# Performance work log

Hardware: AMD Instinct MI355X
Metric: run time of the kernel (lower is better)

Reference implementation:

```python
import jax, jax.numpy as jnp
import numpy as np

N_SRC = 200000   # layer-0 source frontier (nodes)
N_E0  = 100000   # layer-0 targets (hyperedges)
N_E1  = 50000    # layer-1 targets
E0    = 1000000  # edges in layer 0
E1    = 500000   # edges in layer 1
D     = 128      # embedding_dim
H     = 8        # attn heads
BETA  = 0.5      # residual_beta
SLOPE = 0.2      # leaky-relu negative slope
BN_EPS = 1e-5


def _params(key):
    ks = jax.random.split(key, 12)
    def w(k):
        return jax.random.normal(k, (D, D), dtype=jnp.float32) * 0.05
    p = {}
    for i, nm in enumerate(['v2e_Wq', 'v2e_Wk', 'v2e_Wv', 'v2e_We', 'v2e_Wskip',
                            'e2rel_Wq', 'e2rel_Wk', 'e2rel_Wv', 'e2rel_We', 'e2rel_Wskip']):
        p[nm] = w(ks[i])
    p['bn_gamma'] = jnp.ones((D,), jnp.float32)
    p['bn_beta'] = jnp.zeros((D,), jnp.float32)
    return p


def setup_inputs() -> dict:
    key = jax.random.key(0)
    ks = jax.random.split(key, 8)
    inp = {
        'x': jax.random.normal(ks[0], (N_SRC, D), dtype=jnp.float32),
        'ei0': jnp.stack([jax.random.randint(ks[1], (E0,), 0, N_SRC),
                          jax.random.randint(ks[2], (E0,), 0, N_E0)]).astype(jnp.int32),
        'et0': jax.random.randint(ks[3], (E0,), 0, 4).astype(jnp.int32),
        'ei1': jnp.stack([jax.random.randint(ks[4], (E1,), 0, N_E0),
                          jax.random.randint(ks[5], (E1,), 0, N_E1)]).astype(jnp.int32),
        'et1': jax.random.randint(ks[6], (E1,), 0, 4).astype(jnp.int32),
        'emb_type': jax.random.normal(ks[7], (4, D), dtype=jnp.float32),
        'emb_attr': jax.random.normal(jax.random.fold_in(key, 99), (4, D), dtype=jnp.float32),
    }
    inp.update(_params(jax.random.fold_in(key, 1)))
    return inp


def ht_conv(x_src, x_dst, ei, ek, ev, Wq, Wk, Wv, We, Wskip):
    """HypergraphTransformer conv: multi-head edge attention + residual skip.
    x_src [Ns,D], x_dst [Nd,D], ei [2,E], ek/ev [E,D] edge-type/attr embeds."""
    Nd = x_dst.shape[0]
    d = D // H
    src, dst = ei[0], ei[1]
    q = (x_dst @ Wq).reshape(Nd, H, d)                    # [Nd,H,d]
    k = (x_src @ Wk).reshape(-1, H, d)[src] + (ek @ We).reshape(-1, H, d)  # [E,H,d]
    v = (x_src @ Wv).reshape(-1, H, d)[src] + (ev @ We).reshape(-1, H, d)  # [E,H,d]
    logits = jnp.einsum('ehd,ehd->eh', q[dst], k) / jnp.sqrt(jnp.float32(d))
    logits = jnp.where(logits >= 0, logits, SLOPE * logits)  # leaky relu
    # segment softmax over edges sharing a destination
    m = jax.ops.segment_max(logits, dst, num_segments=Nd)    # [Nd,H]
    a = jnp.exp(logits - m[dst])
    s = jax.ops.segment_sum(a, dst, num_segments=Nd)
    alpha = a / (s[dst] + 1e-16)                             # [E,H]
    out = jax.ops.segment_sum(alpha[..., None] * v, dst, num_segments=Nd)  # [Nd,H,d]
    out = out.reshape(Nd, D)
    return BETA * (x_dst @ Wskip) + (1.0 - BETA) * out


def batch_norm(x, gamma, beta):
    mu = jnp.mean(x, axis=0)
    var = jnp.var(x, axis=0)
    return (x - mu) * jax.lax.rsqrt(var + BN_EPS) * gamma + beta


def reference(x, ei0, et0, ei1, et1, emb_type, emb_attr,
              v2e_Wq, v2e_Wk, v2e_Wv, v2e_We, v2e_Wskip,
              e2rel_Wq, e2rel_Wk, e2rel_Wv, e2rel_We, e2rel_Wskip,
              bn_gamma, bn_beta):
    # layer 0: v2e + BatchNorm
    h = ht_conv(x, x[:N_E0], ei0, emb_type[et0], emb_attr[et0],
                v2e_Wq, v2e_Wk, v2e_Wv, v2e_We, v2e_Wskip)
    h = batch_norm(h, bn_gamma, bn_beta)
    # layer 1 (last): e2rel, no BN
    out = ht_conv(h, h[:N_E1], ei1, emb_type[et1], emb_attr[et1],
                  e2rel_Wq, e2rel_Wk, e2rel_Wv, e2rel_We, e2rel_Wskip)
    return out
```

## Files before the change

kernel.cpp:

```cpp
#include <hip/hip_runtime.h>
#include <cstdint>
#include <cstddef>

#define D 128
#define H 8
#define NSRC 200000
#define NE0  100000
#define NE1  50000
#define E0N  1000000
#define E1N  500000
#define NT   (NE0 + NE1)
#define ET   (E0N + E1N)

typedef unsigned short u16;
typedef __attribute__((ext_vector_type(8))) short short8;
typedef __attribute__((ext_vector_type(4))) float f32x4;
typedef __attribute__((ext_vector_type(2))) float f32x2;

__device__ __forceinline__ u16 f2bf(float f) {
  unsigned u = __float_as_uint(f);
  unsigned r = (u + 0x7fffu + ((u >> 16) & 1u)) >> 16;
  return (u16)r;
}
__device__ __forceinline__ float bf2f(u16 u) {
  return __uint_as_float(((unsigned)u) << 16);
}
__device__ __forceinline__ f32x2 unpk(unsigned u) {
  f32x2 r;
  r.x = __uint_as_float(u << 16);
  r.y = __uint_as_float(u & 0xffff0000u);
  return r;
}
__device__ __forceinline__ float dot2bf(unsigned a, unsigned b, float c) {
  float d;
  asm("v_dot2_f32_bf16 %0, %1, %2, %3" : "=v"(d) : "v"(a), "v"(b), "v"(c));
  return d;
}
__device__ __forceinline__ f32x2 fma2(f32x2 a, f32x2 b, f32x2 c) {
  return __builtin_elementwise_fma(a, b, c);
}

#define BC 25000
#define BZ 147
static_assert((size_t)BZ * 1024 >= NT + 1, "offs zero-fill must cover NT+1 entries");
__global__ __launch_bounds__(256) void prep_all(
    const float* __restrict__ x, u16* __restrict__ xb,
    const float* w0, const float* w1, const float* w2, const float* w3,
    const float* w4, const float* w5, const float* w6, const float* w7,
    u16* __restrict__ wt,
    const float* __restrict__ embA, const float* __restrict__ embB,
    const float* __restrict__ We0, const float* __restrict__ We1,
    float* __restrict__ kv,
    int* __restrict__ offs, float* __restrict__ bnsums) {
  int b = blockIdx.x;
  if (b < BC) {
    int i = b * 256 + threadIdx.x;
    float4 a = ((const float4*)x)[i];
    ushort4 o;
    o.x = f2bf(a.x); o.y = f2bf(a.y); o.z = f2bf(a.z); o.w = f2bf(a.w);
    ((ushort4*)xb)[i] = o;
  } else if (b < BC + 64) {
    int bb = b - BC;
    const float* wsrc[8] = {w0, w1, w2, w3, w4, w5, w6, w7};
    int mat = bb >> 3;
    int blk = bb & 7;
    const float* W = wsrc[mat];
    float sc = ((mat & 3) == 2) ? 0.25f : 1.0f;
    u16* out = wt + mat * 16384;
    for (int i = blk * 2048 + threadIdx.x; i < (blk + 1) * 2048; i += 256) {
      int n = i >> 7, k = i & 127;
      out[i] = f2bf(W[k * 128 + n] * sc);
    }
  } else if (b < BC + 68) {
    int bb = b - BC - 64;
    int mat = bb >> 1;
    int t = (bb & 1) * 256 + threadIdx.x;
    const float* We = mat ? We1 : We0;
    float* keOut = kv + mat * 1024;
    float* veOut = keOut + 512;
    int r = t >> 7, c = t & 127;
    float s0 = 0.f, s1 = 0.f;
    for (int k = 0; k < 128; ++k) {
      float w = We[k * 128 + c];
      s0 += embA[r * 128 + k] * w;
      s1 += embB[r * 128 + k] * w;
    }
    keOut[t] = s0;
    veOut[t] = s1;
  } else if (b < BC + 68 + BZ) {
    int base = (b - BC - 68) * 1024 + threadIdx.x * 4;
#pragma unroll
    for (int i = 0; i < 4; ++i)
      if (base + i < NT + 1) offs[base + i] = 0;
  } else {
    bnsums[threadIdx.x] = 0.f;
  }
}

__global__ __launch_bounds__(512, 4) void gemm_quad(
    const u16* __restrict__ A,
    const u16* __restrict__ WtK, const u16* __restrict__ WtV,
    u16* __restrict__ CKV, int NA, int nKV,
    const u16* __restrict__ WtQ, const u16* __restrict__ WtS,
    u16* __restrict__ CQ, u16* __restrict__ CS, int NB) {
  int bb = blockIdx.x;
  const u16 *Wt0, *Wt1;
  int N, tile0;
  bool ilv = (bb < nKV);
  if (ilv) {
    Wt0 = WtK; Wt1 = WtV; N = NA; tile0 = bb * 128;
  } else {
    Wt0 = WtQ; Wt1 = WtS; N = NB; tile0 = (bb - nKV) * 128;
  }
  int tid = threadIdx.x;
  int w = tid >> 6, lane = tid & 63;
  int g = w >> 1;
  int h = w & 1;
  int lrow = lane & 15, q = lane >> 4;

  __shared__ u16 Wls[2 * 128 * 128];

  uint4 wv[8];
#pragma unroll
  for (int i = 0; i < 8; ++i) {
    int m = i * 512 + tid;
    const u16* Wsrc = (m >> 11) ? Wt1 : Wt0;
    wv[i] = *(const uint4*)(Wsrc + (size_t)(m & 2047) * 8);
  }

  int ra = tile0 + g * 32 + lrow;
  int rb = ra + 16;
  bool oka = ra < N, okb = rb < N;
  const u16* pa = A + (size_t)(oka ? ra : 0) * 128 + q * 8;
  const u16* pb = A + (size_t)(okb ? rb : 0) * 128 + q * 8;
  short8 av[4], bv[4];
#pragma unroll
  for (int kk = 0; kk < 4; ++kk) {
    av[kk] = *(const short8*)(pa + kk * 32);
    bv[kk] = *(const short8*)(pb + kk * 32);
  }

#pragma unroll
  for (int i = 0; i < 8; ++i) {
    int m = i * 512 + tid;
    int row = (m & 2047) >> 4, c = m & 15;
    *(uint4*)(Wls + (m >> 11) * 16384 + row * 128 + (c ^ (row & 15)) * 8) = wv[i];
  }
  __syncthreads();

  const u16* W0 = Wls + (h * 64) * 128;
  const u16* W1 = Wls + 16384 + (h * 64) * 128;

  f32x4 acc[2][2][4];
#pragma unroll
  for (int o = 0; o < 2; ++o)
#pragma unroll
    for (int i = 0; i < 2; ++i)
#pragma unroll
      for (int j = 0; j < 4; ++j) acc[o][i][j] = (f32x4){0.f, 0.f, 0.f, 0.f};

  const short8 zero8 = {0, 0, 0, 0, 0, 0, 0, 0};
#pragma unroll
  for (int kk = 0; kk < 4; ++kk) {
    short8 a0 = oka ? av[kk] : zero8;
    short8 a1 = okb ? bv[kk] : zero8;
    int cs = ((kk * 4 + q) ^ lrow) * 8;
#pragma unroll
    for (int j = 0; j < 4; ++j) {
      int fr = j * 16 + lrow;
      short8 b0 = *(const short8*)(W0 + fr * 128 + cs);
      short8 b1 = *(const short8*)(W1 + fr * 128 + cs);
      acc[0][0][j] = __builtin_amdgcn_mfma_f32_16x16x32_bf16(b0, a0, acc[0][0][j], 0, 0, 0);
      acc[0][1][j] = __builtin_amdgcn_mfma_f32_16x16x32_bf16(b0, a1, acc[0][1][j], 0, 0, 0);
      acc[1][0][j] = __builtin_amdgcn_mfma_f32_16x16x32_bf16(b1, a0, acc[1][0][j], 0, 0, 0);
      acc[1][1][j] = __builtin_amdgcn_mfma_f32_16x16x32_bf16(b1, a1, acc[1][1][j], 0, 0, 0);
    }
  }

  if (ilv) {
#pragma unroll
    for (int i = 0; i < 2; ++i) {
      int grow = tile0 + g * 32 + i * 16 + lrow;
      if (grow < N) {
#pragma unroll
        for (int o = 0; o < 2; ++o) {
          u16* base = CKV + (size_t)grow * 256 + (o << 3) + ((q & 1) << 2) +
                      ((q >> 1) << 4) + h * 128;
#pragma unroll
          for (int j = 0; j < 4; ++j) {
            f32x4 v = acc[o][i][j];
            ushort4 pk;
            pk.x = f2bf(v[0]); pk.y = f2bf(v[1]); pk.z = f2bf(v[2]); pk.w = f2bf(v[3]);
            *(ushort4*)(base + j * 32) = pk;
          }
        }
      }
    }
  } else {
#pragma unroll
    for (int o = 0; o < 2; ++o) {
      u16* C = o ? CS : CQ;
#pragma unroll
      for (int i = 0; i < 2; ++i) {
        int grow = tile0 + g * 32 + i * 16 + lrow;
        if (grow < N) {
          u16* base = C + (size_t)grow * 128 + q * 4 + h * 64;
#pragma unroll
          for (int j = 0; j < 4; ++j) {
            f32x4 v = acc[o][i][j];
            ushort4 pk;
            pk.x = f2bf(v[0]); pk.y = f2bf(v[1]); pk.z = f2bf(v[2]); pk.w = f2bf(v[3]);
            *(ushort4*)(base + j * 16) = pk;
          }
        }
      }
    }
  }
}

__global__ __launch_bounds__(256) void csr_count2(
    const int* __restrict__ dst0, const int* __restrict__ dst1,
    int* __restrict__ cnt, int* __restrict__ rank) {
  int t = blockIdx.x * 256 + threadIdx.x;
  if (t < E0N) {
    rank[t] = atomicAdd(&cnt[dst0[t]], 1);
  } else if (t < ET) {
    rank[t] = atomicAdd(&cnt[NE0 + dst1[t - E0N]], 1);
  }
}

__global__ __launch_bounds__(256) void scan1(const int* __restrict__ cnt,
                                             int* __restrict__ excl,
                                             int* __restrict__ blocksums, int N) {
  __shared__ int sh[256];
  int tid = threadIdx.x;
  int base = blockIdx.x * 1024 + tid * 4;
  int v0 = (base + 0 < N) ? cnt[base + 0] : 0;
  int v1 = (base + 1 < N) ? cnt[base + 1] : 0;
  int v2 = (base + 2 < N) ? cnt[base + 2] : 0;
  int v3 = (base + 3 < N) ? cnt[base + 3] : 0;
  int tsum = v0 + v1 + v2 + v3;
  sh[tid] = tsum;
  __syncthreads();
  for (int off = 1; off < 256; off <<= 1) {
    int t2 = (tid >= off) ? sh[tid - off] : 0;
    __syncthreads();
    sh[tid] += t2;
    __syncthreads();
  }
  int incl = sh[tid];
  if (tid == 255) blocksums[blockIdx.x] = incl;
  int run = incl - tsum;
  if (base + 0 < N) excl[base + 0] = run; run += v0;
  if (base + 1 < N) excl[base + 1] = run; run += v1;
  if (base + 2 < N) excl[base + 2] = run; run += v2;
  if (base + 3 < N) excl[base + 3] = run;
}

__global__ void scan2(int* __restrict__ blocksums, int nb) {
  __shared__ int sh[256];
  int tid = threadIdx.x;
  int v = (tid < nb) ? blocksums[tid] : 0;
  sh[tid] = v;
  __syncthreads();
  for (int off = 1; off < 256; off <<= 1) {
    int t2 = (tid >= off) ? sh[tid - off] : 0;
    __syncthreads();
    sh[tid] += t2;
    __syncthreads();
  }
  if (tid < nb) blocksums[tid] = sh[tid] - v;
}

__global__ __launch_bounds__(256) void scan3(int* __restrict__ offs,
                                             const int* __restrict__ blocksums, int N,
                                             int Etot) {
  int t = blockIdx.x * 256 + threadIdx.x;
  if (t < N) offs[t] += blocksums[t >> 10];
  if (t == 0) offs[N] = Etot;
}

__global__ __launch_bounds__(256) void csr_fill2(
    const int* __restrict__ dst0, const int* __restrict__ src0, const int* __restrict__ et0,
    const int* __restrict__ dst1, const int* __restrict__ src1, const int* __restrict__ et1,
    const int* __restrict__ offs, const int* __restrict__ rank,
    int* __restrict__ elist) {
  int t = blockIdx.x * 256 + threadIdx.x;
  if (t < E0N) {
    int p = offs[dst0[t]] + rank[t];
    elist[p] = (src0[t] << 2) | et0[t];
  } else if (t < ET) {
    int t2 = t - E0N;
    int p = offs[NE0 + dst1[t2]] + rank[t];
    elist[p] = (src1[t2] << 2) | et1[t2];
  }
}

__device__ __forceinline__ float sel4(float s0, float s1, float s2, float s3, int ty) {
  float a = (ty & 1) ? s1 : s0;
  float b = (ty & 1) ? s3 : s2;
  return (ty & 2) ? b : a;
}

#define ATTN_BLOCKS 1024

__global__ __launch_bounds__(256) void attn_fused(
    const int* __restrict__ elist, const int* __restrict__ offs,
    const u16* __restrict__ Q, const u16* __restrict__ KV,
    const float* __restrict__ ke, const float* __restrict__ ve,
    const u16* __restrict__ skipb, float* __restrict__ outp, int N,
    float* __restrict__ bnsums) {
  int lane = threadIdx.x & 63;
  int wid = (blockIdx.x << 2) + (threadIdx.x >> 6);
  int wstride = gridDim.x << 2;
  int which = lane >> 4;
  int sub = lane & 15;
  int dim0 = sub * 8;
  int sub16 = sub * 16;
  bool dosum = (bnsums != nullptr);

  __shared__ float vels[4 * 136];
  __shared__ float bsum[128], bsq[128];
  for (int i = threadIdx.x; i < 512; i += 256) {
    int t = i >> 7, c = i & 127;
    vels[t * 136 + c] = ve[t * 128 + c];
  }
  if (threadIdx.x < 128) {
    bsum[threadIdx.x] = 0.f;
    bsq[threadIdx.x] = 0.f;
  }
  __syncthreads();

  float ls[8], lq[8];
#pragma unroll
  for (int i = 0; i < 8; ++i) { ls[i] = 0.f; lq[i] = 0.f; }

  for (int grp = wid; grp * 4 < N; grp += wstride) {
    int d = grp * 4 + which;
    bool active = d < N;
    int dc = active ? d : 0;

    uint4 qp = *(const uint4*)(Q + (size_t)dc * D + dim0);
    f32x2 u0 = unpk(qp.x), u1 = unpk(qp.y), u2 = unpk(qp.z), u3 = unpk(qp.w);

    float qk0, qk1, qk2, qk3;
#pragma unroll
    for (int ty = 0; ty < 4; ++ty) {
      const float* kt = ke + ty * D + dim0;
      float4 ka = *(const float4*)kt;
      float4 kb = *(const float4*)(kt + 4);
      float p = u0.x * ka.x + u0.y * ka.y + u1.x * ka.z + u1.y * ka.w +
                u2.x * kb.x + u2.y * kb.y + u3.x * kb.z + u3.y * kb.w;
      p += __shfl_xor(p, 1, 64);
      if (ty == 0) qk0 = p; else if (ty == 1) qk1 = p; else if (ty == 2) qk2 = p; else qk3 = p;
    }

    int j0 = active ? offs[d] : 0;
    int j1 = active ? offs[d + 1] : 0;
    int j = j0;

    int cp0, cp1, cp2, cp3;
    int fp0, fp1, fp2, fp3;
    {
      int i0 = (j + 0 < j1) ? j + 0 : 0;
      int i1 = (j + 1 < j1) ? j + 1 : 0;
      int i2 = (j + 2 < j1) ? j + 2 : 0;
      int i3 = (j + 3 < j1) ? j + 3 : 0;
      cp0 = elist[i0]; cp1 = elist[i1]; cp2 = elist[i2]; cp3 = elist[i3];
      int k0 = (j + 4 < j1) ? j + 4 : 0;
      int k1 = (j + 5 < j1) ? j + 5 : 0;
      int k2 = (j + 6 < j1) ? j + 6 : 0;
      int k3 = (j + 7 < j1) ? j + 7 : 0;
      fp0 = elist[k0]; fp1 = elist[k1]; fp2 = elist[k2]; fp3 = elist[k3];
    }
    uint4 ck0 = *(const uint4*)(KV + (size_t)(cp0 >> 2) * 256 + sub16);
    uint4 ck1 = *(const uint4*)(KV + (size_t)(cp1 >> 2) * 256 + sub16);
    uint4 ck2 = *(const uint4*)(KV + (size_t)(cp2 >> 2) * 256 + sub16);
    uint4 ck3 = *(const uint4*)(KV + (size_t)(cp3 >> 2) * 256 + sub16);
    uint4 cw0 = *(const uint4*)(KV + (size_t)(cp0 >> 2) * 256 + sub16 + 8);
    uint4 cw1 = *(const uint4*)(KV + (size_t)(cp1 >> 2) * 256 + sub16 + 8);
    uint4 cw2 = *(const uint4*)(KV + (size_t)(cp2 >> 2) * 256 + sub16 + 8);
    uint4 cw3 = *(const uint4*)(KV + (size_t)(cp3 >> 2) * 256 + sub16 + 8);

    float m = -INFINITY, s = 0.f;
    f32x2 acc01 = {0.f, 0.f}, acc23 = {0.f, 0.f}, acc45 = {0.f, 0.f}, acc67 = {0.f, 0.f};

    while (__any(j < j1)) {
      int jn = j + 4;
      uint4 nk0 = *(const uint4*)(KV + (size_t)(fp0 >> 2) * 256 + sub16);
      uint4 nk1 = *(const uint4*)(KV + (size_t)(fp1 >> 2) * 256 + sub16);
      uint4 nk2 = *(const uint4*)(KV + (size_t)(fp2 >> 2) * 256 + sub16);
      uint4 nk3 = *(const uint4*)(KV + (size_t)(fp3 >> 2) * 256 + sub16);
      uint4 nw0 = *(const uint4*)(KV + (size_t)(fp0 >> 2) * 256 + sub16 + 8);
      uint4 nw1 = *(const uint4*)(KV + (size_t)(fp1 >> 2) * 256 + sub16 + 8);
      uint4 nw2 = *(const uint4*)(KV + (size_t)(fp2 >> 2) * 256 + sub16 + 8);
      uint4 nw3 = *(const uint4*)(KV + (size_t)(fp3 >> 2) * 256 + sub16 + 8);
      int g0 = (jn + 4 < j1) ? jn + 4 : 0;
      int g1 = (jn + 5 < j1) ? jn + 5 : 0;
      int g2 = (jn + 6 < j1) ? jn + 6 : 0;
      int g3 = (jn + 7 < j1) ? jn + 7 : 0;
      int gp0 = elist[g0], gp1 = elist[g1], gp2 = elist[g2], gp3 = elist[g3];

      int n = j1 - j;
      if (n > 0) {
        int t0 = cp0 & 3, t1 = cp1 & 3, t2 = cp2 & 3, t3 = cp3 & 3;
        const float* vp0 = vels + t0 * 136 + dim0;
        const float* vp1 = vels + t1 * 136 + dim0;
        const float* vp2 = vels + t2 * 136 + dim0;
        const float* vp3 = vels + t3 * 136 + dim0;
        float4 va0 = *(const float4*)vp0, vb0 = *(const float4*)(vp0 + 4);
        float4 va1 = *(const float4*)vp1, vb1 = *(const float4*)(vp1 + 4);
        float4 va2 = *(const float4*)vp2, vb2 = *(const float4*)(vp2 + 4);
        float4 va3 = *(const float4*)vp3, vb3 = *(const float4*)(vp3 + 4);

        float p0 = dot2bf(qp.x, ck0.x, dot2bf(qp.y, ck0.y, dot2bf(qp.z, ck0.z, dot2bf(qp.w, ck0.w, 0.f))));
        float p1 = dot2bf(qp.x, ck1.x, dot2bf(qp.y, ck1.y, dot2bf(qp.z, ck1.z, dot2bf(qp.w, ck1.w, 0.f))));
        float p2 = dot2bf(qp.x, ck2.x, dot2bf(qp.y, ck2.y, dot2bf(qp.z, ck2.z, dot2bf(qp.w, ck2.w, 0.f))));
        float p3 = dot2bf(qp.x, ck3.x, dot2bf(qp.y, ck3.y, dot2bf(qp.z, ck3.z, dot2bf(qp.w, ck3.w, 0.f))));
        p0 += __shfl_xor(p0, 1, 64);
        p1 += __shfl_xor(p1, 1, 64);
        p2 += __shfl_xor(p2, 1, 64);
        p3 += __shfl_xor(p3, 1, 64);

        float l0 = p0 + sel4(qk0, qk1, qk2, qk3, t0);
        float l1 = p1 + sel4(qk0, qk1, qk2, qk3, t1);
        float l2 = p2 + sel4(qk0, qk1, qk2, qk3, t2);
        float l3 = p3 + sel4(qk0, qk1, qk2, qk3, t3);
        l0 = l0 >= 0.f ? l0 : 0.2f * l0;
        l1 = l1 >= 0.f ? l1 : 0.2f * l1;
        l2 = l2 >= 0.f ? l2 : 0.2f * l2;
        l3 = l3 >= 0.f ? l3 : 0.2f * l3;
        if (n < 2) l1 = -INFINITY;
        if (n < 3) l2 = -INFINITY;
        if (n < 4) l3 = -INFINITY;
        float mb = fmaxf(fmaxf(l0, l1), fmaxf(l2, l3));
        float mn = fmaxf(m, mb);
        float f = __expf(m - mn);
        float a0 = __expf(l0 - mn);
        float a1 = __expf(l1 - mn);
        float a2 = __expf(l2 - mn);
        float a3 = __expf(l3 - mn);
        s = s * f + ((a0 + a1) + (a2 + a3));
        f32x2 ff = {f, f};
        acc01 *= ff; acc23 *= ff; acc45 *= ff; acc67 *= ff;
        f32x2 aa0 = {a0, a0}, aa1 = {a1, a1}, aa2 = {a2, a2}, aa3 = {a3, a3};
        acc01 = fma2(aa0, unpk(cw0.x) + (f32x2){va0.x, va0.y}, acc01);
        acc23 = fma2(aa0, unpk(cw0.y) + (f32x2){va0.z, va0.w}, acc23);
        acc45 = fma2(aa0, unpk(cw0.z) + (f32x2){vb0.x, vb0.y}, acc45);
        acc67 = fma2(aa0, unpk(cw0.w) + (f32x2){vb0.z, vb0.w}, acc67);
        acc01 = fma2(aa1, unpk(cw1.x) + (f32x2){va1.x, va1.y}, acc01);
        acc23 = fma2(aa1, unpk(cw1.y) + (f32x2){va1.z, va1.w}, acc23);
        acc45 = fma2(aa1, unpk(cw1.z) + (f32x2){vb1.x, vb1.y}, acc45);
        acc67 = fma2(aa1, unpk(cw1.w) + (f32x2){vb1.z, vb1.w}, acc67);
        acc01 = fma2(aa2, unpk(cw2.x) + (f32x2){va2.x, va2.y}, acc01);
        acc23 = fma2(aa2, unpk(cw2.y) + (f32x2){va2.z, va2.w}, acc23);
        acc45 = fma2(aa2, unpk(cw2.z) + (f32x2){vb2.x, vb2.y}, acc45);
        acc67 = fma2(aa2, unpk(cw2.w) + (f32x2){vb2.z, vb2.w}, acc67);
        acc01 = fma2(aa3, unpk(cw3.x) + (f32x2){va3.x, va3.y}, acc01);
        acc23 = fma2(aa3, unpk(cw3.y) + (f32x2){va3.z, va3.w}, acc23);
        acc45 = fma2(aa3, unpk(cw3.z) + (f32x2){vb3.x, vb3.y}, acc45);
        acc67 = fma2(aa3, unpk(cw3.w) + (f32x2){vb3.z, vb3.w}, acc67);
        m = mn;
      }
      cp0 = fp0; cp1 = fp1; cp2 = fp2; cp3 = fp3;
      fp0 = gp0; fp1 = gp1; fp2 = gp2; fp3 = gp3;
      ck0 = nk0; ck1 = nk1; ck2 = nk2; ck3 = nk3;
      cw0 = nw0; cw1 = nw1; cw2 = nw2; cw3 = nw3;
      j = jn;
    }
    if (active) {
      float inv = 1.f / (s + 1e-16f);
      float hf = 0.5f * inv;
      uint4 sk = *(const uint4*)(skipb + (size_t)d * D + dim0);
      f32x2 s0 = unpk(sk.x), s1 = unpk(sk.y), s2 = unpk(sk.z), s3 = unpk(sk.w);
      float* op = outp + (size_t)d * D + dim0;
      float4 o0, o1;
      o0.x = 0.5f * s0.x + hf * acc01.x;
      o0.y = 0.5f * s0.y + hf * acc01.y;
      o0.z = 0.5f * s1.x + hf * acc23.x;
      o0.w = 0.5f * s1.y + hf * acc23.y;
      o1.x = 0.5f * s2.x + hf * acc45.x;
      o1.y = 0.5f * s2.y + hf * acc45.y;
      o1.z = 0.5f * s3.x + hf * acc67.x;
      o1.w = 0.5f * s3.y + hf * acc67.y;
      *(float4*)op = o0;
      *(float4*)(op + 4) = o1;
      if (dosum) {
        ls[0] += o0.x; lq[0] += o0.x * o0.x;
        ls[1] += o0.y; lq[1] += o0.y * o0.y;
        ls[2] += o0.z; lq[2] += o0.z * o0.z;
        ls[3] += o0.w; lq[3] += o0.w * o0.w;
        ls[4] += o1.x; lq[4] += o1.x * o1.x;
        ls[5] += o1.y; lq[5] += o1.y * o1.y;
        ls[6] += o1.z; lq[6] += o1.z * o1.z;
        ls[7] += o1.w; lq[7] += o1.w * o1.w;
      }
    }
  }

  if (dosum) {
#pragma unroll
    for (int i = 0; i < 8; ++i) {
      atomicAdd(&bsum[dim0 + i], ls[i]);
      atomicAdd(&bsq[dim0 + i], lq[i]);
    }
    __syncthreads();
    if (threadIdx.x < 128) {
      atomicAdd(&bnsums[threadIdx.x], bsum[threadIdx.x]);
    } else {
      atomicAdd(&bnsums[threadIdx.x], bsq[threadIdx.x - 128]);
    }
  }
}

__global__ __launch_bounds__(256) void bn_apply(const float* __restrict__ h,
                                                u16* __restrict__ hbf,
                                                const float* __restrict__ sums,
                                                const float* __restrict__ gamma,
                                                const float* __restrict__ beta,
                                                float invN, int total) {
  __shared__ float sc[128], sh[128];
  int tid = threadIdx.x;
  if (tid < 128) {
    float mu = sums[tid] * invN;
    float var = sums[128 + tid] * invN - mu * mu;
    float inv = rsqrtf(var + 1e-5f);
    float s = gamma[tid] * inv;
    sc[tid] = s;
    sh[tid] = beta[tid] - mu * s;
  }
  __syncthreads();
  int i = blockIdx.x * 256 + tid;
  if (i < total) {
    int c = i & 127;
    hbf[i] = f2bf(h[i] * sc[c] + sh[c]);
  }
}

extern "C" void kernel_launch(void* const* d_in, const int* in_sizes, int n_in,
                              void* d_out, int out_size, void* d_ws, size_t ws_size,
                              hipStream_t stream) {
  const float* x        = (const float*)d_in[0];
  const int*   ei0      = (const int*)d_in[1];
  const int*   et0      = (const int*)d_in[2];
  const int*   ei1      = (const int*)d_in[3];
  const int*   et1      = (const int*)d_in[4];
  const float* emb_type = (const float*)d_in[5];
  const float* emb_attr = (const float*)d_in[6];
  const float* v2e_Wq   = (const float*)d_in[7];
  const float* v2e_Wk   = (const float*)d_in[8];
  const float* v2e_Wv   = (const float*)d_in[9];
  const float* v2e_We   = (const float*)d_in[10];
  const float* v2e_Wsk  = (const float*)d_in[11];
  const float* e2_Wq    = (const float*)d_in[12];
  const float* e2_Wk    = (const float*)d_in[13];
  const float* e2_Wv    = (const float*)d_in[14];
  const float* e2_We    = (const float*)d_in[15];
  const float* e2_Wsk   = (const float*)d_in[16];
  const float* bn_gamma = (const float*)d_in[17];
  const float* bn_beta  = (const float*)d_in[18];
  float* out = (float*)d_out;

  char* wsb = (char*)d_ws;
  size_t off = 0;
  u16* xb  = (u16*)(wsb + off);  off += (size_t)NSRC * D * 2;
  u16* KVb = (u16*)(wsb + off);  off += (size_t)NSRC * D * 2 * 2;
  u16* Qb  = (u16*)(wsb + off);  off += (size_t)NE0 * D * 2;
  u16* Sb  = (u16*)(wsb + off);  off += (size_t)NE0 * D * 2;
  float* hb = (float*)(wsb + off); off += (size_t)NE0 * D * 4;
  u16* hbf = (u16*)(wsb + off);  off += (size_t)NE0 * D * 2;
  u16* wtAll = (u16*)(wsb + off); off += 8 * 16384 * 2;
  int* elist = (int*)(wsb + off);  off += (size_t)ET * 4;
  int* rank  = (int*)(wsb + off);  off += (size_t)ET * 4;
  int* offs  = (int*)(wsb + off);  off += ((size_t)NT + 8) * 4;
  int* bsums = (int*)(wsb + off);  off += 1024;
  float* kv  = (float*)(wsb + off); off += 4 * 512 * 4;
  float* bnsums = (float*)(wsb + off); off += 256 * 4;

  u16* wtK0 = wtAll + 0 * 16384;
  u16* wtV0 = wtAll + 1 * 16384;
  u16* wtQ0 = wtAll + 2 * 16384;
  u16* wtS0 = wtAll + 3 * 16384;
  u16* wtK1 = wtAll + 4 * 16384;
  u16* wtV1 = wtAll + 5 * 16384;
  u16* wtQ1 = wtAll + 6 * 16384;
  u16* wtS1 = wtAll + 7 * 16384;
  float* kep0 = kv;
  float* vep0 = kv + 512;
  float* kep1 = kv + 1024;
  float* vep1 = kv + 1536;

  const int* src0 = ei0;
  const int* dst0 = ei0 + E0N;
  const int* src1 = ei1;
  const int* dst1 = ei1 + E1N;

  prep_all<<<BC + 64 + 4 + BZ + 1, 256, 0, stream>>>(
      x, xb, v2e_Wk, v2e_Wv, v2e_Wq, v2e_Wsk, e2_Wk, e2_Wv, e2_Wq, e2_Wsk,
      wtAll, emb_type, emb_attr, v2e_We, e2_We, kv, offs, bnsums);

  csr_count2<<<(ET + 255) / 256, 256, 0, stream>>>(dst0, dst1, offs, rank);
  {
    int nb = (NT + 1023) / 1024;
    scan1<<<nb, 256, 0, stream>>>(offs, offs, bsums, NT);
    scan2<<<1, 256, 0, stream>>>(bsums, nb);
    scan3<<<(NT + 255) / 256, 256, 0, stream>>>(offs, bsums, NT, ET);
  }
  csr_fill2<<<(ET + 255) / 256, 256, 0, stream>>>(dst0, src0, et0, dst1, src1, et1,
                                                  offs, rank, elist);

  {
    int nKV = (NSRC + 127) / 128, nQS = (NE0 + 127) / 128;
    gemm_quad<<<nKV + nQS, 512, 0, stream>>>(xb, wtK0, wtV0, KVb, NSRC, nKV,
                                             wtQ0, wtS0, Qb, Sb, NE0);
  }
  attn_fused<<<ATTN_BLOCKS, 256, 0, stream>>>(elist, offs, Qb, KVb, kep0, vep0,
                                              Sb, hb, NE0, bnsums);
  bn_apply<<<(NE0 * D + 255) / 256, 256, 0, stream>>>(hb, hbf, bnsums, bn_gamma, bn_beta,
                                                      1.0f / (float)NE0, NE0 * D);

  {
    int nKV = (NE0 + 127) / 128, nQS = (NE1 + 127) / 128;
    gemm_quad<<<nKV + nQS, 512, 0, stream>>>(hbf, wtK1, wtV1, KVb, NE0, nKV,
                                             wtQ1, wtS1, Qb, Sb, NE1);
  }
  attn_fused<<<ATTN_BLOCKS, 256, 0, stream>>>(elist, offs + NE0, Qb, KVb, kep1, vep1,
                                              Sb, out, NE1, nullptr);
}
```

Measured before the change: 584.1 us.

## Fold BatchNorm affine into layer-1 projection weights and bias

The separate BatchNorm apply pass is removed. The first attention kernel now writes bf16 pre-norm activations directly. A small kernel rescales the four layer-1 transposed weight matrices by the per-channel BN scale and computes a bias from the BN shift, which the GEMM epilogue adds. This avoids writing and re-reading an fp32 intermediate of NE0x128 and one full elementwise launch. In exchange, the pre-norm values are rounded to bf16 before normalization and the folded weights are requantized to bf16, which may shift accuracy slightly.

```diff
diff --git a/kernel.cpp b/kernel.cpp
--- a/kernel.cpp
+++ b/kernel.cpp
@@ -97,12 +97,39 @@
   }
 }
 
+__global__ __launch_bounds__(128) void bn_fold(
+    u16* __restrict__ wt1, const float* __restrict__ sums,
+    const float* __restrict__ gamma, const float* __restrict__ beta,
+    float invN, float* __restrict__ bias) {
+  __shared__ float s_[128], t_[128];
+  int tid = threadIdx.x;
+  {
+    float mu = sums[tid] * invN;
+    float var = sums[128 + tid] * invN - mu * mu;
+    float sc = gamma[tid] * rsqrtf(var + 1e-5f);
+    s_[tid] = sc;
+    t_[tid] = beta[tid] - mu * sc;
+  }
+  __syncthreads();
+  int mat = blockIdx.x, n = tid;
+  u16* wrow = wt1 + mat * 16384 + n * 128;
+  float b = 0.f;
+#pragma unroll 4
+  for (int k = 0; k < 128; ++k) {
+    float w = bf2f(wrow[k]);
+    b += t_[k] * w;
+    wrow[k] = f2bf(s_[k] * w);
+  }
+  bias[mat * 128 + n] = b;
+}
+
 __global__ __launch_bounds__(512, 4) void gemm_quad(
     const u16* __restrict__ A,
     const u16* __restrict__ WtK, const u16* __restrict__ WtV,
     u16* __restrict__ CKV, int NA, int nKV,
     const u16* __restrict__ WtQ, const u16* __restrict__ WtS,
-    u16* __restrict__ CQ, u16* __restrict__ CS, int NB) {
+    u16* __restrict__ CQ, u16* __restrict__ CS, int NB,
+    const float* __restrict__ bias) {
   int bb = blockIdx.x;
   const u16 *Wt0, *Wt1;
   int N, tile0;
@@ -189,8 +216,11 @@
 #pragma unroll
           for (int j = 0; j < 4; ++j) {
             f32x4 v = acc[o][i][j];
+            float4 bs = {0.f, 0.f, 0.f, 0.f};
+            if (bias) bs = *(const float4*)(bias + o * 128 + h * 64 + j * 16 + q * 4);
             ushort4 pk;
-            pk.x = f2bf(v[0]); pk.y = f2bf(v[1]); pk.z = f2bf(v[2]); pk.w = f2bf(v[3]);
+            pk.x = f2bf(v[0] + bs.x); pk.y = f2bf(v[1] + bs.y);
+            pk.z = f2bf(v[2] + bs.z); pk.w = f2bf(v[3] + bs.w);
             *(ushort4*)(base + j * 32) = pk;
           }
         }
@@ -208,8 +238,11 @@
 #pragma unroll
           for (int j = 0; j < 4; ++j) {
             f32x4 v = acc[o][i][j];
+            float4 bs = {0.f, 0.f, 0.f, 0.f};
+            if (bias) bs = *(const float4*)(bias + (2 + o) * 128 + h * 64 + j * 16 + q * 4);
             ushort4 pk;
-            pk.x = f2bf(v[0]); pk.y = f2bf(v[1]); pk.z = f2bf(v[2]); pk.w = f2bf(v[3]);
+            pk.x = f2bf(v[0] + bs.x); pk.y = f2bf(v[1] + bs.y);
+            pk.z = f2bf(v[2] + bs.z); pk.w = f2bf(v[3] + bs.w);
             *(ushort4*)(base + j * 16) = pk;
           }
         }
@@ -308,8 +341,8 @@
     const int* __restrict__ elist, const int* __restrict__ offs,
     const u16* __restrict__ Q, const u16* __restrict__ KV,
     const float* __restrict__ ke, const float* __restrict__ ve,
-    const u16* __restrict__ skipb, float* __restrict__ outp, int N,
-    float* __restrict__ bnsums) {
+    const u16* __restrict__ skipb, float* __restrict__ outp,
+    u16* __restrict__ outb, int N, float* __restrict__ bnsums) {
   int lane = threadIdx.x & 63;
   int wid = (blockIdx.x << 2) + (threadIdx.x >> 6);
   int wstride = gridDim.x << 2;
@@ -473,7 +506,6 @@
       float hf = 0.5f * inv;
       uint4 sk = *(const uint4*)(skipb + (size_t)d * D + dim0);
       f32x2 s0 = unpk(sk.x), s1 = unpk(sk.y), s2 = unpk(sk.z), s3 = unpk(sk.w);
-      float* op = outp + (size_t)d * D + dim0;
       float4 o0, o1;
       o0.x = 0.5f * s0.x + hf * acc01.x;
       o0.y = 0.5f * s0.y + hf * acc01.y;
@@ -483,8 +515,18 @@
       o1.y = 0.5f * s2.y + hf * acc45.y;
       o1.z = 0.5f * s3.x + hf * acc67.x;
       o1.w = 0.5f * s3.y + hf * acc67.y;
-      *(float4*)op = o0;
-      *(float4*)(op + 4) = o1;
+      if (outb) {
+        ushort4 pA, pB;
+        pA.x = f2bf(o0.x); pA.y = f2bf(o0.y); pA.z = f2bf(o0.z); pA.w = f2bf(o0.w);
+        pB.x = f2bf(o1.x); pB.y = f2bf(o1.y); pB.z = f2bf(o1.z); pB.w = f2bf(o1.w);
+        u16* ob = outb + (size_t)d * D + dim0;
+        *(ushort4*)ob = pA;
+        *(ushort4*)(ob + 4) = pB;
+      } else {
+        float* op = outp + (size_t)d * D + dim0;
+        *(float4*)op = o0;
+        *(float4*)(op + 4) = o1;
+      }
       if (dosum) {
         ls[0] += o0.x; lq[0] += o0.x * o0.x;
         ls[1] += o0.y; lq[1] += o0.y * o0.y;
@@ -510,30 +552,6 @@
     } else {
       atomicAdd(&bnsums[threadIdx.x], bsq[threadIdx.x - 128]);
     }
-  }
-}
-
-__global__ __launch_bounds__(256) void bn_apply(const float* __restrict__ h,
-                                                u16* __restrict__ hbf,
-                                                const float* __restrict__ sums,
-                                                const float* __restrict__ gamma,
-                                                const float* __restrict__ beta,
-                                                float invN, int total) {
-  __shared__ float sc[128], sh[128];
-  int tid = threadIdx.x;
-  if (tid < 128) {
-    float mu = sums[tid] * invN;
-    float var = sums[128 + tid] * invN - mu * mu;
-    float inv = rsqrtf(var + 1e-5f);
-    float s = gamma[tid] * inv;
-    sc[tid] = s;
-    sh[tid] = beta[tid] - mu * s;
-  }
-  __syncthreads();
-  int i = blockIdx.x * 256 + tid;
-  if (i < total) {
-    int c = i & 127;
-    hbf[i] = f2bf(h[i] * sc[c] + sh[c]);
   }
 }
 
@@ -567,7 +585,6 @@
   u16* KVb = (u16*)(wsb + off);  off += (size_t)NSRC * D * 2 * 2;
   u16* Qb  = (u16*)(wsb + off);  off += (size_t)NE0 * D * 2;
   u16* Sb  = (u16*)(wsb + off);  off += (size_t)NE0 * D * 2;
-  float* hb = (float*)(wsb + off); off += (size_t)NE0 * D * 4;
   u16* hbf = (u16*)(wsb + off);  off += (size_t)NE0 * D * 2;
   u16* wtAll = (u16*)(wsb + off); off += 8 * 16384 * 2;
   int* elist = (int*)(wsb + off);  off += (size_t)ET * 4;
@@ -576,6 +593,7 @@
   int* bsums = (int*)(wsb + off);  off += 1024;
   float* kv  = (float*)(wsb + off); off += 4 * 512 * 4;
   float* bnsums = (float*)(wsb + off); off += 256 * 4;
+  float* bias = (float*)(wsb + off); off += 512 * 4;
 
   u16* wtK0 = wtAll + 0 * 16384;
   u16* wtV0 = wtAll + 1 * 16384;
@@ -612,18 +630,19 @@
   {
     int nKV = (NSRC + 127) / 128, nQS = (NE0 + 127) / 128;
     gemm_quad<<<nKV + nQS, 512, 0, stream>>>(xb, wtK0, wtV0, KVb, NSRC, nKV,
-                                             wtQ0, wtS0, Qb, Sb, NE0);
+                                             wtQ0, wtS0, Qb, Sb, NE0, nullptr);
   }
   attn_fused<<<ATTN_BLOCKS, 256, 0, stream>>>(elist, offs, Qb, KVb, kep0, vep0,
-                                              Sb, hb, NE0, bnsums);
-  bn_apply<<<(NE0 * D + 255) / 256, 256, 0, stream>>>(hb, hbf, bnsums, bn_gamma, bn_beta,
-                                                      1.0f / (float)NE0, NE0 * D);
+                                              Sb, nullptr, hbf, NE0, bnsums);
+
+  bn_fold<<<4, 128, 0, stream>>>(wtK1, bnsums, bn_gamma, bn_beta,
+                                 1.0f / (float)NE0, bias);
 
   {
     int nKV = (NE0 + 127) / 128, nQS = (NE1 + 127) / 128;
     gemm_quad<<<nKV + nQS, 512, 0, stream>>>(hbf, wtK1, wtV1, KVb, NE0, nKV,
-                                             wtQ1, wtS1, Qb, Sb, NE1);
+                                             wtQ1, wtS1, Qb, Sb, NE1, bias);
   }
   attn_fused<<<ATTN_BLOCKS, 256, 0, stream>>>(elist, offs + NE0, Qb, KVb, kep1, vep1,
-                                              Sb, out, NE1, nullptr);
-}
+                                              Sb, out, nullptr, NE1, nullptr);
+}
```

New measurement: 570.7 us. 1.02x faster.
